# Kernel tuning notes

Measured on AMD Instinct MI355X. Metric: run time of the kernel, lower is better.

Reference implementation:

```python
import jax, jax.numpy as jnp
import numpy as np

B, H, W, C = 16, 32, 32, 256
N = H * W


def setup_inputs() -> dict:
    key = jax.random.key(0)
    ks = jax.random.split(key, 8)
    x = jax.random.normal(ks[0], (B, H, W, C), dtype=jnp.float32)
    # nn.LazyLinear(C): weight (C, C), bias (C,)
    scale = 1.0 / np.sqrt(C)
    Wq = jax.random.uniform(ks[1], (C, C), jnp.float32, -scale, scale)
    bq = jax.random.uniform(ks[2], (C,), jnp.float32, -scale, scale)
    Wk = jax.random.uniform(ks[3], (C, C), jnp.float32, -scale, scale)
    bk = jax.random.uniform(ks[4], (C,), jnp.float32, -scale, scale)
    Wv = jax.random.uniform(ks[5], (C, C), jnp.float32, -scale, scale)
    bv = jax.random.uniform(ks[6], (C,), jnp.float32, -scale, scale)
    # torch.randn(H, H*W, W)
    Wp = jax.random.normal(ks[7], (H, N, W), dtype=jnp.float32)
    return {"x": x, "Wq": Wq, "bq": bq, "Wk": Wk, "bk": bk,
            "Wv": Wv, "bv": bv, "Wp": Wp}


def reference(x, Wq, bq, Wk, bk, Wv, bv, Wp):
    b, h, w, c = x.shape
    n = h * w
    # Linear projections (torch Linear: x @ W^T + b), flatten spatial dims to N tokens
    q = (jnp.einsum('bhwc,dc->bhwd', x, Wq) + bq).reshape(b, n, c)
    k = (jnp.einsum('bhwc,dc->bhwd', x, Wk) + bk).reshape(b, n, c)
    v = (jnp.einsum('bhwc,dc->bhwd', x, Wv) + bv).reshape(b, n, c)
    # Unscaled attention over the N spatial tokens (no 1/sqrt(C) in the original)
    scores = jnp.einsum('bnc,bmc->bnm', q, k)          # (B, N, N)
    attn = jax.nn.softmax(scores, axis=-1)
    qkv = jnp.einsum('bnm,bmc->bnc', attn, v)           # (B, N, C)
    # z = (qkv^T [B,1,C,N] @ Wp [H,N,W]).transpose(-2,-1) -> (B, H, W, C)
    z = jnp.einsum('bnc,hnw->bhwc', qkv, Wp)
    return z
```

## Files before the change

### kernel.cpp

```cpp
#include <hip/hip_runtime.h>
#include <hip/hip_bf16.h>

#define BB 16
#define NN 1024
#define CC 256

typedef __attribute__((ext_vector_type(8))) short bf16x8;
typedef __attribute__((ext_vector_type(4))) short s16x4;
typedef __attribute__((ext_vector_type(4))) float f32x4;

#define GPTR(p) ((const __attribute__((address_space(1))) void*)(p))
#define LPTR(p) ((__attribute__((address_space(3))) void*)(p))

__device__ __forceinline__ unsigned short f2bf(float f) {
  union { float f; unsigned u; } v; v.f = f;
  unsigned r = v.u + 0x7FFFu + ((v.u >> 16) & 1u);
  return (unsigned short)(r >> 16);
}

__device__ __forceinline__ bf16x8 pack8(f32x4 a, f32x4 b) {
  bf16x8 o;
  o[0] = (short)f2bf(a[0]); o[1] = (short)f2bf(a[1]);
  o[2] = (short)f2bf(a[2]); o[3] = (short)f2bf(a[3]);
  o[4] = (short)f2bf(b[0]); o[5] = (short)f2bf(b[1]);
  o[6] = (short)f2bf(b[2]); o[7] = (short)f2bf(b[3]);
  return o;
}

template <int BIAS_MODE, int F32OUT>
__global__ __launch_bounds__(256) void gemm_tile(
    const unsigned short* __restrict__ A, int lda, long sA,
    const unsigned short* __restrict__ Bt, int ldb, long sB,
    const float* __restrict__ bias,
    void* __restrict__ Out, int ldo, long sO, int K) {
  __shared__ unsigned short As[2][2 * 128 * 32];
  __shared__ unsigned short Bs[2][2 * 64 * 32];
  int b = blockIdx.x;
  int m0 = blockIdx.y * 128;
  int n0 = blockIdx.z * 64;
  int t = threadIdx.x;
  int w = t >> 6, lane = t & 63;
  int wm = (w >> 1) * 64, wn = (w & 1) * 32;
  int r = lane & 15, g = lane >> 4;

  const unsigned short* Ab = A + (long)b * sA;
  const unsigned short* Bb = Bt + (long)b * sB;

  int srow = t >> 2;
  int scol = (t & 3) * 8;

  f32x4 acc[4][2];
#pragma unroll
  for (int i = 0; i < 4; i++)
#pragma unroll
    for (int j = 0; j < 2; j++) acc[i][j] = (f32x4){0.f, 0.f, 0.f, 0.f};

#define STAGE_GT(buf, k0)                                                     \
  do {                                                                        \
    _Pragma("unroll") for (int kh = 0; kh < 2; kh++) {                        \
      _Pragma("unroll") for (int jj = 0; jj < 2; jj++) {                      \
        __builtin_amdgcn_global_load_lds(                                     \
            GPTR(Ab + (long)(m0 + srow + jj * 64) * lda + (k0) + kh * 32 +    \
                 scol),                                                       \
            LPTR(&As[buf][kh * 4096 + jj * 2048 + t * 8]), 16, 0, 0);         \
      }                                                                       \
      __builtin_amdgcn_global_load_lds(                                       \
          GPTR(Bb + (long)(n0 + srow) * ldb + (k0) + kh * 32 + scol),         \
          LPTR(&Bs[buf][kh * 2048 + t * 8]), 16, 0, 0);                       \
    }                                                                         \
  } while (0)

  int nt = K >> 6;
  STAGE_GT(0, 0);
  for (int tt = 0; tt < nt; ++tt) {
    int cb = tt & 1;
    if (tt < nt - 1) {
      STAGE_GT(cb ^ 1, (tt + 1) * 64);
      asm volatile("s_waitcnt vmcnt(6)" ::: "memory");
    } else {
      asm volatile("s_waitcnt vmcnt(0)" ::: "memory");
    }
    __builtin_amdgcn_sched_barrier(0);
    __builtin_amdgcn_s_barrier();
    __builtin_amdgcn_sched_barrier(0);
#pragma unroll
    for (int kh = 0; kh < 2; kh++) {
      bf16x8 af[4], bfr[2];
#pragma unroll
      for (int ti = 0; ti < 4; ti++)
        af[ti] = *(const bf16x8*)&As[cb][kh * 4096 + (wm + ti * 16 + r) * 32 + g * 8];
#pragma unroll
      for (int tj = 0; tj < 2; tj++)
        bfr[tj] = *(const bf16x8*)&Bs[cb][kh * 2048 + (wn + tj * 16 + r) * 32 + g * 8];
#pragma unroll
      for (int ti = 0; ti < 4; ti++)
#pragma unroll
        for (int tj = 0; tj < 2; tj++)
          acc[ti][tj] = __builtin_amdgcn_mfma_f32_16x16x32_bf16(af[ti], bfr[tj], acc[ti][tj], 0, 0, 0);
    }
    __builtin_amdgcn_s_barrier();
  }
#undef STAGE_GT

#pragma unroll
  for (int ti = 0; ti < 4; ti++) {
#pragma unroll
    for (int tj = 0; tj < 2; tj++) {
      int col = n0 + wn + tj * 16 + r;
      float bc = (BIAS_MODE == 1) ? bias[col] : 0.0f;
#pragma unroll
      for (int rr = 0; rr < 4; rr++) {
        int row = m0 + wm + ti * 16 + g * 4 + rr;
        float val = acc[ti][tj][rr] + bc;
        long oidx = (long)b * sO + (long)row * ldo + col;
        if (F32OUT)
          ((float*)Out)[oidx] = val;
        else
          ((unsigned short*)Out)[oidx] = f2bf(val);
      }
    }
  }
}

__global__ __launch_bounds__(256) void gemm_qkv(
    const float* __restrict__ x,
    const float* __restrict__ Wq, const float* __restrict__ Wk,
    const float* __restrict__ Wv,
    const float* __restrict__ bq, const float* __restrict__ bk,
    const float* __restrict__ bv,
    const float* __restrict__ Wp,
    unsigned short* __restrict__ Qb, unsigned short* __restrict__ Kb,
    unsigned short* __restrict__ Vtb, unsigned short* __restrict__ Amat) {
  __shared__ unsigned short As[2 * 128 * 32];
  __shared__ unsigned short Bs[2 * 128 * 32];
  __shared__ float tile[32][33];

  if (blockIdx.z == 6) {
    int id = blockIdx.x * 8 + blockIdx.y;
#pragma unroll 1
    for (int u = 0; u < 8; u++) {
      int wb = id * 8 + u;
      int h = wb >> 5;
      int n0w = (wb & 31) * 32;
#pragma unroll
      for (int j = 0; j < 4; j++) {
        int idx = threadIdx.x + j * 256;
        int a = idx >> 5, wc = idx & 31;
        tile[a][wc] = Wp[(size_t)h * (NN * 32) + (size_t)(n0w + a) * 32 + wc];
      }
      __syncthreads();
#pragma unroll
      for (int j = 0; j < 4; j++) {
        int idx = threadIdx.x + j * 256;
        int wc = idx >> 5, a = idx & 31;
        Amat[(size_t)(h * 32 + wc) * NN + n0w + a] = f2bf(tile[a][wc]);
      }
      __syncthreads();
    }
    return;
  }

  int b = blockIdx.x;
  int m0 = blockIdx.y * 128;
  int n0 = blockIdx.z * 128;
  int t = threadIdx.x;
  int w = t >> 6, lane = t & 63;
  int wm = (w >> 1) * 64, wn = (w & 1) * 64;
  int r = lane & 15, g = lane >> 4;

  const float* Ab = x + (long)b * NN * CC;
  int srow = t >> 2;
  int scol = (t & 3) * 8;

  const float* Wsel[2];
  int wrow[2];
#pragma unroll
  for (int jj = 0; jj < 2; jj++) {
    int nbase = n0 + jj * 64;
    int seg = nbase >> 8;
    Wsel[jj] = (seg == 0) ? Wq : (seg == 1 ? Wk : Wv);
    wrow[jj] = (nbase + srow) & 255;
  }

  f32x4 acc[4][4];
#pragma unroll
  for (int i = 0; i < 4; i++)
#pragma unroll
    for (int j = 0; j < 4; j++) acc[i][j] = (f32x4){0.f, 0.f, 0.f, 0.f};

  f32x4 pa[4][2], pw[4][2];
#pragma unroll
  for (int kh = 0; kh < 2; kh++)
#pragma unroll
    for (int jj = 0; jj < 2; jj++) {
      const float* asrc = Ab + (long)(m0 + srow + jj * 64) * CC + kh * 32 + scol;
      pa[kh * 2 + jj][0] = *(const f32x4*)asrc;
      pa[kh * 2 + jj][1] = *(const f32x4*)(asrc + 4);
      const float* wsrc = Wsel[jj] + (long)wrow[jj] * CC + kh * 32 + scol;
      pw[kh * 2 + jj][0] = *(const f32x4*)wsrc;
      pw[kh * 2 + jj][1] = *(const f32x4*)(wsrc + 4);
    }

  for (int k0 = 0; k0 < CC; k0 += 64) {
    if (k0) __builtin_amdgcn_s_barrier();
#pragma unroll
    for (int kh = 0; kh < 2; kh++)
#pragma unroll
      for (int jj = 0; jj < 2; jj++) {
        *(bf16x8*)&As[kh * 4096 + jj * 2048 + t * 8] =
            pack8(pa[kh * 2 + jj][0], pa[kh * 2 + jj][1]);
        *(bf16x8*)&Bs[kh * 4096 + jj * 2048 + t * 8] =
            pack8(pw[kh * 2 + jj][0], pw[kh * 2 + jj][1]);
      }
    if (k0 < CC - 64) {
#pragma unroll
      for (int kh = 0; kh < 2; kh++)
#pragma unroll
        for (int jj = 0; jj < 2; jj++) {
          const float* asrc =
              Ab + (long)(m0 + srow + jj * 64) * CC + k0 + 64 + kh * 32 + scol;
          pa[kh * 2 + jj][0] = *(const f32x4*)asrc;
          pa[kh * 2 + jj][1] = *(const f32x4*)(asrc + 4);
          const float* wsrc =
              Wsel[jj] + (long)wrow[jj] * CC + k0 + 64 + kh * 32 + scol;
          pw[kh * 2 + jj][0] = *(const f32x4*)wsrc;
          pw[kh * 2 + jj][1] = *(const f32x4*)(wsrc + 4);
        }
    }
    asm volatile("s_waitcnt lgkmcnt(0)" ::: "memory");
    __builtin_amdgcn_sched_barrier(0);
    __builtin_amdgcn_s_barrier();
    __builtin_amdgcn_sched_barrier(0);
#pragma unroll
    for (int kh = 0; kh < 2; kh++) {
      bf16x8 af[4], bfr[4];
#pragma unroll
      for (int ti = 0; ti < 4; ti++)
        af[ti] = *(const bf16x8*)&As[kh * 4096 + (wm + ti * 16 + r) * 32 + g * 8];
#pragma unroll
      for (int tj = 0; tj < 4; tj++)
        bfr[tj] = *(const bf16x8*)&Bs[kh * 4096 + (wn + tj * 16 + r) * 32 + g * 8];
#pragma unroll
      for (int ti = 0; ti < 4; ti++)
#pragma unroll
        for (int tj = 0; tj < 4; tj++)
          acc[ti][tj] = __builtin_amdgcn_mfma_f32_16x16x32_bf16(af[ti], bfr[tj], acc[ti][tj], 0, 0, 0);
    }
  }

  int sege = (n0 + wn) >> 8;
  const float* bsel = (sege == 0) ? bq : (sege == 1 ? bk : bv);
  int seg = n0 >> 8;
#pragma unroll
  for (int ti = 0; ti < 4; ti++) {
#pragma unroll
    for (int tj = 0; tj < 4; tj++) {
      int col = n0 + wn + tj * 16 + r;
      int c = col & 255;
      float bc = bsel[c];
#pragma unroll
      for (int rr = 0; rr < 4; rr++) {
        int row = m0 + wm + ti * 16 + g * 4 + rr;
        float val = acc[ti][tj][rr] + bc;
        long base = (long)b * NN * CC;
        if (seg == 0) {
          Qb[base + (long)row * CC + c] = f2bf(val);
        } else if (seg == 1) {
          Kb[base + ((long)(c >> 5) * NN + row) * 32 + (c & 31)] = f2bf(val);
        } else {
          Vtb[base + ((((long)(c >> 4) * 128 + (row >> 3)) * 16 + (c & 15)) * 8 + (row & 7))] = f2bf(val);
        }
      }
    }
  }
}

__global__ __launch_bounds__(512, 2) void attn_fused(
    const unsigned short* __restrict__ Q,
    const unsigned short* __restrict__ Kt,
    const unsigned short* __restrict__ Vt,
    unsigned short* __restrict__ QKVt) {
  __shared__ unsigned short ShBuf[64 * 1024];
  __shared__ float red[8][64];
  int b = blockIdx.x;
  int n0 = blockIdx.y * 64;
  int t = threadIdx.x;
  int w = t >> 6, lane = t & 63;
  int r = lane & 15, g = lane >> 4;

  const unsigned short* kslab = Kt + (long)b * NN * CC + w * 128 * 32;
  unsigned short* wbuf0 = &ShBuf[w * 4096];
  unsigned short* wbuf1 = &ShBuf[32768 + w * 4096];

  const unsigned short* qbase = Q + ((long)b * NN + n0 + r) * CC + g * 8;

#pragma unroll
  for (int j = 0; j < 8; j++)
    __builtin_amdgcn_global_load_lds(GPTR(kslab + j * 512 + lane * 8),
                                     LPTR(wbuf0 + j * 512 + lane * 8), 16, 0, 0);
  bf16x8 qa[4];
#pragma unroll
  for (int rt = 0; rt < 4; rt++)
    qa[rt] = *(const bf16x8*)(qbase + rt * 16 * CC);

  f32x4 acc[4][8];
#pragma unroll
  for (int i = 0; i < 4; i++)
#pragma unroll
    for (int j = 0; j < 8; j++) acc[i][j] = (f32x4){0.f, 0.f, 0.f, 0.f};

#pragma unroll
  for (int kk = 0; kk < 8; kk++) {
    unsigned short* cur = (kk & 1) ? wbuf1 : wbuf0;
    unsigned short* nxt = (kk & 1) ? wbuf0 : wbuf1;
    if (kk < 7) {
      const unsigned short* src = kslab + (long)(kk + 1) * (NN * 32);
#pragma unroll
      for (int j = 0; j < 8; j++)
        __builtin_amdgcn_global_load_lds(GPTR(src + j * 512 + lane * 8),
                                         LPTR(nxt + j * 512 + lane * 8), 16, 0, 0);
      asm volatile("s_waitcnt vmcnt(8)" ::: "memory");
    } else {
      asm volatile("s_waitcnt vmcnt(0)" ::: "memory");
    }
    __builtin_amdgcn_sched_barrier(0);
    bf16x8 qn[4];
    if (kk < 7) {
#pragma unroll
      for (int rt = 0; rt < 4; rt++)
        qn[rt] = *(const bf16x8*)(qbase + (kk + 1) * 32 + rt * 16 * CC);
    }
    __builtin_amdgcn_s_setprio(1);
#pragma unroll
    for (int ct = 0; ct < 8; ct++) {
      bf16x8 kf = *(const bf16x8*)&cur[(ct * 16 + r) * 32 + g * 8];
#pragma unroll
      for (int rt = 0; rt < 4; rt++)
        acc[rt][ct] = __builtin_amdgcn_mfma_f32_16x16x32_bf16(qa[rt], kf, acc[rt][ct], 0, 0, 0);
    }
    __builtin_amdgcn_s_setprio(0);
    if (kk < 7) {
#pragma unroll
      for (int rt = 0; rt < 4; rt++) qa[rt] = qn[rt];
    }
    __builtin_amdgcn_sched_barrier(0);
  }

  const unsigned short* vbase = Vt + (long)b * NN * CC;
  int cw = w * 32;
  bf16x8 brp[2];
#pragma unroll
  for (int bt = 0; bt < 2; bt++) {
    long vidx = (((long)((cw >> 4) + bt) * 128 + g) * 16 + r) * 8;
    brp[bt] = *(const bf16x8*)(vbase + vidx);
  }
  __builtin_amdgcn_sched_barrier(0);

  float mrow[4][4];
#pragma unroll
  for (int rt = 0; rt < 4; rt++) {
#pragma unroll
    for (int rr = 0; rr < 4; rr++) {
      float m = acc[rt][0][rr];
#pragma unroll
      for (int ct = 1; ct < 8; ct++) m = fmaxf(m, acc[rt][ct][rr]);
#pragma unroll
      for (int d = 1; d < 16; d <<= 1) m = fmaxf(m, __shfl_xor(m, d, 64));
      mrow[rt][rr] = m;
    }
  }
  if (r == 0) {
#pragma unroll
    for (int rt = 0; rt < 4; rt++)
#pragma unroll
      for (int rr = 0; rr < 4; rr++)
        red[w][rt * 16 + g * 4 + rr] = mrow[rt][rr];
  }
  __syncthreads();
#pragma unroll
  for (int rt = 0; rt < 4; rt++) {
#pragma unroll
    for (int rr = 0; rr < 4; rr++) {
      int row = rt * 16 + g * 4 + rr;
      float m = red[0][row];
#pragma unroll
      for (int w2 = 1; w2 < 8; w2++) m = fmaxf(m, red[w2][row]);
      mrow[rt][rr] = m;
    }
  }
  __syncthreads();
  float ssum[4][4];
#pragma unroll
  for (int rt = 0; rt < 4; rt++) {
#pragma unroll
    for (int rr = 0; rr < 4; rr++) {
      float s = 0.f;
#pragma unroll
      for (int ct = 0; ct < 8; ct++) {
        float e = exp2f((acc[rt][ct][rr] - mrow[rt][rr]) * 1.44269504088896f);
        acc[rt][ct][rr] = e;
        s += e;
      }
#pragma unroll
      for (int d = 1; d < 16; d <<= 1) s += __shfl_xor(s, d, 64);
      ssum[rt][rr] = s;
    }
  }
  if (r == 0) {
#pragma unroll
    for (int rt = 0; rt < 4; rt++)
#pragma unroll
      for (int rr = 0; rr < 4; rr++)
        red[w][rt * 16 + g * 4 + rr] = ssum[rt][rr];
  }
  __syncthreads();
#pragma unroll
  for (int rt = 0; rt < 4; rt++) {
#pragma unroll
    for (int rr = 0; rr < 4; rr++) {
      int prow = rt * 16 + g * 4 + rr;
      float s = 0.f;
#pragma unroll
      for (int w2 = 0; w2 < 8; w2++) s += red[w2][prow];
      float inv = 1.0f / s;
      int sw = prow & 7;
#pragma unroll
      for (int ct = 0; ct < 8; ct++) {
        int col = w * 128 + ct * 16 + r;
        int chunk = (col >> 3) ^ sw;
        ShBuf[prow * 1024 + chunk * 8 + (col & 7)] = f2bf(acc[rt][ct][rr] * inv);
      }
    }
  }
  __syncthreads();

  f32x4 o[4][2];
#pragma unroll
  for (int i = 0; i < 4; i++)
#pragma unroll
    for (int j = 0; j < 2; j++) o[i][j] = (f32x4){0.f, 0.f, 0.f, 0.f};

#pragma unroll 4
  for (int m0 = 0; m0 < NN; m0 += 32) {
    bf16x8 ar[4], br[2];
    br[0] = brp[0]; br[1] = brp[1];
    if (m0 + 32 < NN) {
#pragma unroll
      for (int bt = 0; bt < 2; bt++) {
        long vidx = (((long)((cw >> 4) + bt) * 128 + ((m0 + 32) >> 3) + g) * 16 + r) * 8;
        brp[bt] = *(const bf16x8*)(vbase + vidx);
      }
    }
#pragma unroll
    for (int rt = 0; rt < 4; rt++) {
      int prow = rt * 16 + r;
      int chunk = ((m0 >> 3) + g) ^ (prow & 7);
      ar[rt] = *(const bf16x8*)&ShBuf[prow * 1024 + chunk * 8];
    }
    __builtin_amdgcn_s_setprio(1);
#pragma unroll
    for (int rt = 0; rt < 4; rt++)
#pragma unroll
      for (int bt = 0; bt < 2; bt++)
        o[rt][bt] = __builtin_amdgcn_mfma_f32_16x16x32_bf16(ar[rt], br[bt], o[rt][bt], 0, 0, 0);
    __builtin_amdgcn_s_setprio(0);
  }

  unsigned short* obase = QKVt + (long)b * NN * CC;
#pragma unroll
  for (int rt = 0; rt < 4; rt++) {
#pragma unroll
    for (int bt = 0; bt < 2; bt++) {
      int c = cw + bt * 16 + r;
      int n = n0 + rt * 16 + g * 4;
      s16x4 pk;
      pk.x = (short)f2bf(o[rt][bt][0]);
      pk.y = (short)f2bf(o[rt][bt][1]);
      pk.z = (short)f2bf(o[rt][bt][2]);
      pk.w = (short)f2bf(o[rt][bt][3]);
      *(s16x4*)(obase + (long)c * NN + n) = pk;
    }
  }
}

extern "C" void kernel_launch(void* const* d_in, const int* in_sizes, int n_in,
                              void* d_out, int out_size, void* d_ws, size_t ws_size,
                              hipStream_t stream) {
  const float* x  = (const float*)d_in[0];
  const float* Wq = (const float*)d_in[1];
  const float* bq = (const float*)d_in[2];
  const float* Wk = (const float*)d_in[3];
  const float* bk = (const float*)d_in[4];
  const float* Wv = (const float*)d_in[5];
  const float* bv = (const float*)d_in[6];
  const float* Wp = (const float*)d_in[7];
  float* out = (float*)d_out;

  const long BNC = (long)BB * NN * CC;

  char* p = (char*)d_ws;
  unsigned short* Amat  = (unsigned short*)p; p += (long)NN * NN * 2;
  unsigned short* Qb    = (unsigned short*)p; p += BNC * 2;
  unsigned short* Ktb   = (unsigned short*)p; p += BNC * 2;
  unsigned short* Vtb   = (unsigned short*)p; p += BNC * 2;
  unsigned short* QKVt  = (unsigned short*)p; p += BNC * 2;

  gemm_qkv<<<dim3(BB, 8, 7), 256, 0, stream>>>(
      x, Wq, Wk, Wv, bq, bk, bv, Wp, Qb, Ktb, Vtb, Amat);

  attn_fused<<<dim3(BB, NN / 64), 512, 0, stream>>>(Qb, Ktb, Vtb, QKVt);

  gemm_tile<0, 1><<<dim3(BB, 8, 4), 256, 0, stream>>>(
      Amat, NN, 0L, QKVt, NN, (long)NN * CC, nullptr,
      out, CC, (long)NN * CC, NN);
}
```

Measured before the change: 149.9 us.

## Split attention block across 16 waves with swizzled K tiles and transposed MFMA

```diff
diff --git a/kernel.cpp b/kernel.cpp
--- a/kernel.cpp
+++ b/kernel.cpp
@@ -275,51 +275,58 @@
   }
 }
 
-__global__ __launch_bounds__(512, 2) void attn_fused(
+__global__ __launch_bounds__(1024, 4) void attn_fused(
     const unsigned short* __restrict__ Q,
     const unsigned short* __restrict__ Kt,
     const unsigned short* __restrict__ Vt,
     unsigned short* __restrict__ QKVt) {
   __shared__ unsigned short ShBuf[64 * 1024];
-  __shared__ float red[8][64];
+  __shared__ float red_m[64][20];
+  __shared__ float red_s[64][20];
   int b = blockIdx.x;
   int n0 = blockIdx.y * 64;
   int t = threadIdx.x;
   int w = t >> 6, lane = t & 63;
   int r = lane & 15, g = lane >> 4;
 
-  const unsigned short* kslab = Kt + (long)b * NN * CC + w * 128 * 32;
-  unsigned short* wbuf0 = &ShBuf[w * 4096];
-  unsigned short* wbuf1 = &ShBuf[32768 + w * 4096];
+  const unsigned short* kslab = Kt + (long)b * NN * CC;
+  unsigned short* buf0 = &ShBuf[0];
+  unsigned short* buf1 = &ShBuf[32 * 1024];
+
+  int stok = w * 64 + (lane >> 2);
+  int sgrp = (lane & 3) ^ ((lane >> 2) & 3);
+  const unsigned short* ksrc0 = kslab + (long)stok * 32 + sgrp * 8;
+  int dbase = (w * 64) * 32 + lane * 8;
+
+#pragma unroll
+  for (int i = 0; i < 4; i++)
+    __builtin_amdgcn_global_load_lds(GPTR(ksrc0 + i * 512),
+                                     LPTR(&buf0[dbase + i * 512]), 16, 0, 0);
 
   const unsigned short* qbase = Q + ((long)b * NN + n0 + r) * CC + g * 8;
-
-#pragma unroll
-  for (int j = 0; j < 8; j++)
-    __builtin_amdgcn_global_load_lds(GPTR(kslab + j * 512 + lane * 8),
-                                     LPTR(wbuf0 + j * 512 + lane * 8), 16, 0, 0);
   bf16x8 qa[4];
 #pragma unroll
   for (int rt = 0; rt < 4; rt++)
     qa[rt] = *(const bf16x8*)(qbase + rt * 16 * CC);
 
-  f32x4 acc[4][8];
+  f32x4 acc[4][4];
 #pragma unroll
   for (int i = 0; i < 4; i++)
 #pragma unroll
-    for (int j = 0; j < 8; j++) acc[i][j] = (f32x4){0.f, 0.f, 0.f, 0.f};
-
+    for (int j = 0; j < 4; j++) acc[i][j] = (f32x4){0.f, 0.f, 0.f, 0.f};
+
+  int kgrp = (g ^ (r & 3)) * 8;
 #pragma unroll
   for (int kk = 0; kk < 8; kk++) {
-    unsigned short* cur = (kk & 1) ? wbuf1 : wbuf0;
-    unsigned short* nxt = (kk & 1) ? wbuf0 : wbuf1;
+    unsigned short* cur = (kk & 1) ? buf1 : buf0;
+    unsigned short* nxt = (kk & 1) ? buf0 : buf1;
     if (kk < 7) {
-      const unsigned short* src = kslab + (long)(kk + 1) * (NN * 32);
-#pragma unroll
-      for (int j = 0; j < 8; j++)
-        __builtin_amdgcn_global_load_lds(GPTR(src + j * 512 + lane * 8),
-                                         LPTR(nxt + j * 512 + lane * 8), 16, 0, 0);
-      asm volatile("s_waitcnt vmcnt(8)" ::: "memory");
+      const unsigned short* src = ksrc0 + (long)(kk + 1) * (NN * 32);
+#pragma unroll
+      for (int i = 0; i < 4; i++)
+        __builtin_amdgcn_global_load_lds(GPTR(src + i * 512),
+                                         LPTR(&nxt[dbase + i * 512]), 16, 0, 0);
+      asm volatile("s_waitcnt vmcnt(4)" ::: "memory");
     } else {
       asm volatile("s_waitcnt vmcnt(0)" ::: "memory");
     }
@@ -332,11 +339,11 @@
     }
     __builtin_amdgcn_s_setprio(1);
 #pragma unroll
-    for (int ct = 0; ct < 8; ct++) {
-      bf16x8 kf = *(const bf16x8*)&cur[(ct * 16 + r) * 32 + g * 8];
+    for (int ct = 0; ct < 4; ct++) {
+      bf16x8 kf = *(const bf16x8*)&cur[(w * 64 + ct * 16 + r) * 32 + kgrp];
 #pragma unroll
       for (int rt = 0; rt < 4; rt++)
-        acc[rt][ct] = __builtin_amdgcn_mfma_f32_16x16x32_bf16(qa[rt], kf, acc[rt][ct], 0, 0, 0);
+        acc[rt][ct] = __builtin_amdgcn_mfma_f32_16x16x32_bf16(kf, qa[rt], acc[rt][ct], 0, 0, 0);
     }
     __builtin_amdgcn_s_setprio(0);
     if (kk < 7) {
@@ -347,110 +354,95 @@
   }
 
   const unsigned short* vbase = Vt + (long)b * NN * CC;
-  int cw = w * 32;
-  bf16x8 brp[2];
-#pragma unroll
-  for (int bt = 0; bt < 2; bt++) {
-    long vidx = (((long)((cw >> 4) + bt) * 128 + g) * 16 + r) * 8;
-    brp[bt] = *(const bf16x8*)(vbase + vidx);
-  }
+  bf16x8 brp = *(const bf16x8*)(vbase + (((long)w * 128 + g) * 16 + r) * 8);
   __builtin_amdgcn_sched_barrier(0);
 
-  float mrow[4][4];
+  float mrow[4];
 #pragma unroll
   for (int rt = 0; rt < 4; rt++) {
-#pragma unroll
-    for (int rr = 0; rr < 4; rr++) {
-      float m = acc[rt][0][rr];
-#pragma unroll
-      for (int ct = 1; ct < 8; ct++) m = fmaxf(m, acc[rt][ct][rr]);
-#pragma unroll
-      for (int d = 1; d < 16; d <<= 1) m = fmaxf(m, __shfl_xor(m, d, 64));
-      mrow[rt][rr] = m;
-    }
-  }
-  if (r == 0) {
-#pragma unroll
-    for (int rt = 0; rt < 4; rt++)
-#pragma unroll
-      for (int rr = 0; rr < 4; rr++)
-        red[w][rt * 16 + g * 4 + rr] = mrow[rt][rr];
+    float m = acc[rt][0][0];
+#pragma unroll
+    for (int ct = 0; ct < 4; ct++)
+#pragma unroll
+      for (int rr = 0; rr < 4; rr++) m = fmaxf(m, acc[rt][ct][rr]);
+    m = fmaxf(m, __shfl_xor(m, 16, 64));
+    m = fmaxf(m, __shfl_xor(m, 32, 64));
+    mrow[rt] = m;
+  }
+  if (lane < 16) {
+#pragma unroll
+    for (int rt = 0; rt < 4; rt++) red_m[rt * 16 + lane][w] = mrow[rt];
   }
   __syncthreads();
 #pragma unroll
   for (int rt = 0; rt < 4; rt++) {
-#pragma unroll
-    for (int rr = 0; rr < 4; rr++) {
-      int row = rt * 16 + g * 4 + rr;
-      float m = red[0][row];
-#pragma unroll
-      for (int w2 = 1; w2 < 8; w2++) m = fmaxf(m, red[w2][row]);
-      mrow[rt][rr] = m;
-    }
-  }
-  __syncthreads();
-  float ssum[4][4];
+    int row = rt * 16 + r;
+    f32x4 a = *(const f32x4*)&red_m[row][0];
+    f32x4 bq4 = *(const f32x4*)&red_m[row][4];
+    f32x4 c = *(const f32x4*)&red_m[row][8];
+    f32x4 d = *(const f32x4*)&red_m[row][12];
+    float m = fmaxf(fmaxf(fmaxf(a[0], a[1]), fmaxf(a[2], a[3])),
+                    fmaxf(fmaxf(bq4[0], bq4[1]), fmaxf(bq4[2], bq4[3])));
+    m = fmaxf(m, fmaxf(fmaxf(fmaxf(c[0], c[1]), fmaxf(c[2], c[3])),
+                       fmaxf(fmaxf(d[0], d[1]), fmaxf(d[2], d[3]))));
+    mrow[rt] = m;
+  }
+  float ssum[4];
 #pragma unroll
   for (int rt = 0; rt < 4; rt++) {
-#pragma unroll
-    for (int rr = 0; rr < 4; rr++) {
-      float s = 0.f;
-#pragma unroll
-      for (int ct = 0; ct < 8; ct++) {
-        float e = exp2f((acc[rt][ct][rr] - mrow[rt][rr]) * 1.44269504088896f);
+    float s = 0.f;
+#pragma unroll
+    for (int ct = 0; ct < 4; ct++)
+#pragma unroll
+      for (int rr = 0; rr < 4; rr++) {
+        float e = exp2f((acc[rt][ct][rr] - mrow[rt]) * 1.44269504088896f);
         acc[rt][ct][rr] = e;
         s += e;
       }
-#pragma unroll
-      for (int d = 1; d < 16; d <<= 1) s += __shfl_xor(s, d, 64);
-      ssum[rt][rr] = s;
-    }
-  }
-  if (r == 0) {
-#pragma unroll
-    for (int rt = 0; rt < 4; rt++)
-#pragma unroll
-      for (int rr = 0; rr < 4; rr++)
-        red[w][rt * 16 + g * 4 + rr] = ssum[rt][rr];
+    s += __shfl_xor(s, 16, 64);
+    s += __shfl_xor(s, 32, 64);
+    ssum[rt] = s;
+  }
+  if (lane < 16) {
+#pragma unroll
+    for (int rt = 0; rt < 4; rt++) red_s[rt * 16 + lane][w] = ssum[rt];
   }
   __syncthreads();
 #pragma unroll
   for (int rt = 0; rt < 4; rt++) {
-#pragma unroll
-    for (int rr = 0; rr < 4; rr++) {
-      int prow = rt * 16 + g * 4 + rr;
-      float s = 0.f;
-#pragma unroll
-      for (int w2 = 0; w2 < 8; w2++) s += red[w2][prow];
-      float inv = 1.0f / s;
-      int sw = prow & 7;
-#pragma unroll
-      for (int ct = 0; ct < 8; ct++) {
-        int col = w * 128 + ct * 16 + r;
-        int chunk = (col >> 3) ^ sw;
-        ShBuf[prow * 1024 + chunk * 8 + (col & 7)] = f2bf(acc[rt][ct][rr] * inv);
-      }
+    int prow = rt * 16 + r;
+    f32x4 a = *(const f32x4*)&red_s[prow][0];
+    f32x4 bq4 = *(const f32x4*)&red_s[prow][4];
+    f32x4 c = *(const f32x4*)&red_s[prow][8];
+    f32x4 d = *(const f32x4*)&red_s[prow][12];
+    float s = (a[0] + a[1] + a[2] + a[3]) + (bq4[0] + bq4[1] + bq4[2] + bq4[3]) +
+              (c[0] + c[1] + c[2] + c[3]) + (d[0] + d[1] + d[2] + d[3]);
+    float inv = 1.0f / s;
+    int sw = prow & 7;
+#pragma unroll
+    for (int ct = 0; ct < 4; ct++) {
+      int col = w * 64 + ct * 16 + g * 4;
+      int chunk = (col >> 3) ^ sw;
+      s16x4 pk;
+      pk.x = (short)f2bf(acc[rt][ct][0] * inv);
+      pk.y = (short)f2bf(acc[rt][ct][1] * inv);
+      pk.z = (short)f2bf(acc[rt][ct][2] * inv);
+      pk.w = (short)f2bf(acc[rt][ct][3] * inv);
+      *(s16x4*)&ShBuf[prow * 1024 + chunk * 8 + (col & 7)] = pk;
     }
   }
   __syncthreads();
 
-  f32x4 o[4][2];
-#pragma unroll
-  for (int i = 0; i < 4; i++)
-#pragma unroll
-    for (int j = 0; j < 2; j++) o[i][j] = (f32x4){0.f, 0.f, 0.f, 0.f};
+  f32x4 o[4];
+#pragma unroll
+  for (int i = 0; i < 4; i++) o[i] = (f32x4){0.f, 0.f, 0.f, 0.f};
 
 #pragma unroll 4
   for (int m0 = 0; m0 < NN; m0 += 32) {
-    bf16x8 ar[4], br[2];
-    br[0] = brp[0]; br[1] = brp[1];
-    if (m0 + 32 < NN) {
-#pragma unroll
-      for (int bt = 0; bt < 2; bt++) {
-        long vidx = (((long)((cw >> 4) + bt) * 128 + ((m0 + 32) >> 3) + g) * 16 + r) * 8;
-        brp[bt] = *(const bf16x8*)(vbase + vidx);
-      }
-    }
+    bf16x8 ar[4], br;
+    br = brp;
+    if (m0 + 32 < NN)
+      brp = *(const bf16x8*)(vbase + (((long)w * 128 + ((m0 + 32) >> 3) + g) * 16 + r) * 8);
 #pragma unroll
     for (int rt = 0; rt < 4; rt++) {
       int prow = rt * 16 + r;
@@ -460,26 +452,21 @@
     __builtin_amdgcn_s_setprio(1);
 #pragma unroll
     for (int rt = 0; rt < 4; rt++)
-#pragma unroll
-      for (int bt = 0; bt < 2; bt++)
-        o[rt][bt] = __builtin_amdgcn_mfma_f32_16x16x32_bf16(ar[rt], br[bt], o[rt][bt], 0, 0, 0);
+      o[rt] = __builtin_amdgcn_mfma_f32_16x16x32_bf16(ar[rt], br, o[rt], 0, 0, 0);
     __builtin_amdgcn_s_setprio(0);
   }
 
   unsigned short* obase = QKVt + (long)b * NN * CC;
+  int c = w * 16 + r;
 #pragma unroll
   for (int rt = 0; rt < 4; rt++) {
-#pragma unroll
-    for (int bt = 0; bt < 2; bt++) {
-      int c = cw + bt * 16 + r;
-      int n = n0 + rt * 16 + g * 4;
-      s16x4 pk;
-      pk.x = (short)f2bf(o[rt][bt][0]);
-      pk.y = (short)f2bf(o[rt][bt][1]);
-      pk.z = (short)f2bf(o[rt][bt][2]);
-      pk.w = (short)f2bf(o[rt][bt][3]);
-      *(s16x4*)(obase + (long)c * NN + n) = pk;
-    }
+    int n = n0 + rt * 16 + g * 4;
+    s16x4 pk;
+    pk.x = (short)f2bf(o[rt][0]);
+    pk.y = (short)f2bf(o[rt][1]);
+    pk.z = (short)f2bf(o[rt][2]);
+    pk.w = (short)f2bf(o[rt][3]);
+    *(s16x4*)(obase + (long)c * NN + n) = pk;
   }
 }
 
@@ -508,7 +495,7 @@
   gemm_qkv<<<dim3(BB, 8, 7), 256, 0, stream>>>(
       x, Wq, Wk, Wv, bq, bk, bv, Wp, Qb, Ktb, Vtb, Amat);
 
-  attn_fused<<<dim3(BB, NN / 64), 512, 0, stream>>>(Qb, Ktb, Vtb, QKVt);
+  attn_fused<<<dim3(BB, NN / 64), 1024, 0, stream>>>(Qb, Ktb, Vtb, QKVt);
 
   gemm_tile<0, 1><<<dim3(BB, 8, 4), 256, 0, stream>>>(
       Amat, NN, 0L, QKVt, NN, (long)NN * CC, nullptr,
```

Result: slower. 155.6 us (+3.8%).
